# Kernel optimization log

Measured on AMD Instinct MI355X. Metric: run time of the kernel, lower is better.

Reference implementation:

```python
import jax, jax.numpy as jnp
import numpy as np

B, T, C = 2, 2048, 2048
H = 16
ROPE_DIM, NOPE_DIM, V_DIM = 64, 64, 128
HEAD_DIM = NOPE_DIM + ROPE_DIM  # 128
Q_RANK, KV_RANK = 1536, 512


def setup_inputs() -> dict:
    key = jax.random.key(0)
    ks = jax.random.split(key, 8)
    std = 0.02
    return {
        "x": jax.random.normal(ks[0], (B, T, C), jnp.float32),
        "cos": jax.random.normal(ks[1], (1, T, 1, ROPE_DIM // 2), jnp.float32),
        "sin": jax.random.normal(ks[2], (1, T, 1, ROPE_DIM // 2), jnp.float32),
        "wq_down": jax.random.normal(ks[3], (Q_RANK, C), jnp.float32) * std,
        "wq_up": jax.random.normal(ks[4], (H * HEAD_DIM, Q_RANK), jnp.float32) * std,
        "wkv_down": jax.random.normal(ks[5], (KV_RANK, C), jnp.float32) * std,
        "wkv_up": jax.random.normal(ks[6], (H * (HEAD_DIM + V_DIM), KV_RANK), jnp.float32) * std,
        "wo": jax.random.normal(ks[7], (C, H * V_DIM), jnp.float32) * std,
    }


def _rope(x, cos, sin):
    # x: [B, T, H, rope_dim]
    d = x.shape[-1] // 2
    x1, x2 = x[..., :d], x[..., d:]
    return jnp.concatenate([x1 * cos + x2 * sin, -x1 * sin + x2 * cos], axis=-1)


def _rms_norm(x):
    eps = jnp.finfo(x.dtype).eps
    return x * jax.lax.rsqrt(jnp.mean(jnp.square(x), axis=-1, keepdims=True) + eps)


def reference(x, cos, sin, wq_down, wq_up, wkv_down, wkv_up, wo):
    # Low-rank q projection
    q = jnp.einsum('btc,rc,dr->btd', x, wq_down, wq_up)
    q = q.reshape(B, T, H, HEAD_DIM)
    q_nope, q_rope = q[..., :NOPE_DIM], q[..., NOPE_DIM:]
    # Low-rank kv projection (naive decompression)
    kv = jnp.einsum('btc,rc,dr->btd', x, wkv_down, wkv_up)
    kv = kv.reshape(B, T, H, HEAD_DIM + V_DIM)
    k_nope = kv[..., :NOPE_DIM]
    k_rope = kv[..., NOPE_DIM:HEAD_DIM]
    v = kv[..., HEAD_DIM:]
    # Partial RoPE on the rope sub-dims only
    q_rope = _rope(q_rope, cos, sin)
    k_rope = _rope(k_rope, cos, sin)
    q = _rms_norm(jnp.concatenate([q_nope, q_rope], axis=-1))
    k = _rms_norm(jnp.concatenate([k_nope, k_rope], axis=-1))
    # Causal SDPA: [B, H, T, T]
    scale = 1.0 / jnp.sqrt(jnp.float32(HEAD_DIM))
    scores = jnp.einsum('bthd,bshd->bhts', q, k) * scale
    causal = jnp.tril(jnp.ones((T, T), dtype=bool))
    scores = jnp.where(causal, scores, jnp.finfo(scores.dtype).min)
    probs = jax.nn.softmax(scores, axis=-1)
    y = jnp.einsum('bhts,bshd->bthd', probs, v).reshape(B, T, H * V_DIM)
    return y @ wo.T
```

## Files before the change

kernel.cpp:

```cpp
#include <hip/hip_runtime.h>
#include <hip/hip_bf16.h>
#include <math.h>
#include <type_traits>

#define AS1 __attribute__((address_space(1)))
#define AS3 __attribute__((address_space(3)))

typedef __bf16  bf16x8 __attribute__((ext_vector_type(8)));
typedef float   f32x4  __attribute__((ext_vector_type(4)));
typedef __hip_bfloat16 bf16;

#define MFMA16x16x32 __builtin_amdgcn_mfma_f32_16x16x32_bf16

__device__ __forceinline__ void gload16(const void* g, void* l) {
  __builtin_amdgcn_global_load_lds((const AS1 void*)g, (AS3 void*)l, 16, 0, 0);
}

__device__ __forceinline__ unsigned short bfbits(float v) {
  return __builtin_bit_cast(unsigned short, __float2bfloat16(v));
}

struct CastArgs {
  const float4* src[6];
  ushort4* dst[6];
  unsigned bound[6];
};

__global__ __launch_bounds__(256) void f2bf_multi(CastArgs a) {
  unsigned i = blockIdx.x * 256 + threadIdx.x;
  if (i >= a.bound[5]) return;
  unsigned lo = 0;
  int s = 0;
#pragma unroll
  for (int k = 0; k < 5; k++) {
    if (i >= a.bound[k]) { s = k + 1; lo = a.bound[k]; }
  }
  unsigned idx = i - lo;
  float4 v = a.src[s][idx];
  ushort4 o;
  o.x = bfbits(v.x); o.y = bfbits(v.y); o.z = bfbits(v.z); o.w = bfbits(v.w);
  a.dst[s][idx] = o;
}

template <typename OutT>
__global__ __launch_bounds__(256, 3) void gemm_bt64(const bf16* __restrict__ A,
                                                    const bf16* __restrict__ W,
                                                    OutT* __restrict__ Cp,
                                                    int N, int K, int lda) {
  __shared__ __align__(16) bf16 As[128 * 64];
  __shared__ __align__(16) bf16 Ws[128 * 64];
  const int t = threadIdx.x;
  const int w = t >> 6, lane = t & 63;
  const int quad = lane >> 4, l16 = lane & 15;
  const int wr = (w >> 1) * 64, wc = (w & 1) * 64;
  const unsigned bid = blockIdx.x, nwg = gridDim.x;
  const unsigned swz = (bid & 7) * (nwg >> 3) + (bid >> 3);
  const size_t m0 = (size_t)(swz & 31) * 128;
  const size_t n0 = (size_t)(swz >> 5) * 128;

  const int r8 = lane >> 3;
  const int cg = (lane & 7) ^ r8;
  const bf16* aSrc = A + (m0 + w * 8 + r8) * (size_t)lda + cg * 8;
  const bf16* wSrc = W + (n0 + w * 8 + r8) * (size_t)K + cg * 8;
  const size_t sA = (size_t)32 * lda, sW = (size_t)32 * K;

  const int cx0 = ((quad) ^ (l16 & 7)) << 4;
  const int cx1 = ((4 + quad) ^ (l16 & 7)) << 4;
  const char* aRb = (const char*)As + (wr + l16) * 128;
  const char* bRb = (const char*)Ws + (wc + l16) * 128;

  f32x4 acc[4][4];
#pragma unroll
  for (int i = 0; i < 4; i++)
#pragma unroll
    for (int j = 0; j < 4; j++) acc[i][j] = f32x4{0.f, 0.f, 0.f, 0.f};

  for (int k0 = 0; k0 < K; k0 += 64) {
    __syncthreads();
#pragma unroll
    for (int is = 0; is < 4; ++is)
      gload16(aSrc + is * sA, (char*)As + is * 4096 + w * 1024);
#pragma unroll
    for (int is = 0; is < 4; ++is)
      gload16(wSrc + is * sW, (char*)Ws + is * 4096 + w * 1024);
    aSrc += 64; wSrc += 64;
    __syncthreads();

    bf16x8 af[4][2], bw[4][2];
#pragma unroll
    for (int i = 0; i < 4; i++) {
      af[i][0] = *(const bf16x8*)(aRb + i * 2048 + cx0);
      af[i][1] = *(const bf16x8*)(aRb + i * 2048 + cx1);
    }
#pragma unroll
    for (int j = 0; j < 4; j++) {
      bw[j][0] = *(const bf16x8*)(bRb + j * 2048 + cx0);
      bw[j][1] = *(const bf16x8*)(bRb + j * 2048 + cx1);
    }
    __builtin_amdgcn_s_setprio(1);
#pragma unroll
    for (int i = 0; i < 4; i++)
#pragma unroll
      for (int j = 0; j < 4; j++)
#pragma unroll
        for (int ks = 0; ks < 2; ks++)
          acc[i][j] = MFMA16x16x32(af[i][ks], bw[j][ks], acc[i][j], 0, 0, 0);
    __builtin_amdgcn_s_setprio(0);
  }

#pragma unroll
  for (int i = 0; i < 4; i++)
#pragma unroll
    for (int j = 0; j < 4; j++)
#pragma unroll
      for (int r = 0; r < 4; r++) {
        size_t row = m0 + wr + i * 16 + quad * 4 + r;
        size_t col = n0 + wc + j * 16 + l16;
        float v = acc[i][j][r];
        if constexpr (std::is_same<OutT, float>::value)
          Cp[row * N + col] = v;
        else
          Cp[row * N + col] = __float2bfloat16(v);
      }
}

__global__ __launch_bounds__(256, 3) void gemm_kvup64(const bf16* __restrict__ A,
                                                      const bf16* __restrict__ W,
                                                      bf16* __restrict__ kvraw,
                                                      bf16* __restrict__ vT) {
  __shared__ __align__(16) bf16 As[128 * 64];
  __shared__ __align__(16) bf16 Ws[128 * 64];
  const int t = threadIdx.x;
  const int w = t >> 6, lane = t & 63;
  const int quad = lane >> 4, l16 = lane & 15;
  const int wr = (w >> 1) * 64, wc = (w & 1) * 64;
  const int K = 512, lda = 2048;
  const unsigned bid = blockIdx.x, nwg = gridDim.x;
  const unsigned swz = (bid & 7) * (nwg >> 3) + (bid >> 3);
  const size_t m0 = (size_t)(swz & 31) * 128;
  const int n0 = (int)(swz >> 5) * 128;

  const int r8 = lane >> 3;
  const int cg = (lane & 7) ^ r8;
  const bf16* aSrc = A + (m0 + w * 8 + r8) * (size_t)lda + cg * 8;
  const bf16* wSrc = W + ((size_t)n0 + w * 8 + r8) * (size_t)K + cg * 8;
  const size_t sA = (size_t)32 * lda, sW = (size_t)32 * K;

  const int cx0 = ((quad) ^ (l16 & 7)) << 4;
  const int cx1 = ((4 + quad) ^ (l16 & 7)) << 4;
  const char* aRb = (const char*)As + (wr + l16) * 128;
  const char* bRb = (const char*)Ws + (wc + l16) * 128;

  f32x4 acc[4][4];
#pragma unroll
  for (int i = 0; i < 4; i++)
#pragma unroll
    for (int j = 0; j < 4; j++) acc[i][j] = f32x4{0.f, 0.f, 0.f, 0.f};

  for (int k0 = 0; k0 < K; k0 += 64) {
    __syncthreads();
#pragma unroll
    for (int is = 0; is < 4; ++is)
      gload16(aSrc + is * sA, (char*)As + is * 4096 + w * 1024);
#pragma unroll
    for (int is = 0; is < 4; ++is)
      gload16(wSrc + is * sW, (char*)Ws + is * 4096 + w * 1024);
    aSrc += 64; wSrc += 64;
    __syncthreads();

    bf16x8 af[4][2], bw[4][2];
#pragma unroll
    for (int i = 0; i < 4; i++) {
      af[i][0] = *(const bf16x8*)(aRb + i * 2048 + cx0);
      af[i][1] = *(const bf16x8*)(aRb + i * 2048 + cx1);
    }
#pragma unroll
    for (int j = 0; j < 4; j++) {
      bw[j][0] = *(const bf16x8*)(bRb + j * 2048 + cx0);
      bw[j][1] = *(const bf16x8*)(bRb + j * 2048 + cx1);
    }
    __builtin_amdgcn_s_setprio(1);
#pragma unroll
    for (int i = 0; i < 4; i++)
#pragma unroll
      for (int j = 0; j < 4; j++)
#pragma unroll
        for (int ks = 0; ks < 2; ks++)
          acc[i][j] = MFMA16x16x32(af[i][ks], bw[j][ks], acc[i][j], 0, 0, 0);
    __builtin_amdgcn_s_setprio(0);
  }

  if ((n0 & 128) == 0) {
#pragma unroll
    for (int i = 0; i < 4; i++)
#pragma unroll
      for (int j = 0; j < 4; j++)
#pragma unroll
        for (int r = 0; r < 4; r++) {
          size_t row = m0 + wr + i * 16 + quad * 4 + r;
          size_t col = (size_t)n0 + wc + j * 16 + l16;
          kvraw[row * 4096 + col] = __float2bfloat16(acc[i][j][r]);
        }
  } else {
    const int h = n0 >> 8;
#pragma unroll
    for (int i = 0; i < 4; i++) {
      size_t row = m0 + wr + i * 16 + quad * 4;
      int bb = (int)(row >> 11), tloc = (int)(row & 2047);
#pragma unroll
      for (int j = 0; j < 4; j++) {
        int d = wc + j * 16 + l16;
        ushort4 v4;
        v4.x = bfbits(acc[i][j][0]);
        v4.y = bfbits(acc[i][j][1]);
        v4.z = bfbits(acc[i][j][2]);
        v4.w = bfbits(acc[i][j][3]);
        *(ushort4*)(vT + ((size_t)(bb * 16 + h) * 128 + d) * 2048 + tloc) = v4;
      }
    }
  }
}

__global__ __launch_bounds__(256) void rope_rms(const bf16* __restrict__ qraw,
                                                const bf16* __restrict__ kvraw,
                                                const float* __restrict__ cosp,
                                                const float* __restrict__ sinp,
                                                bf16* __restrict__ qn,
                                                bf16* __restrict__ kn) {
  const int bt = blockIdx.x;
  const int w = threadIdx.x >> 6, lane = threadIdx.x & 63;
  const int h = blockIdx.y * 4 + w;
  const int tt = bt & 2047;
  const float c = cosp[tt * 32 + (lane & 31)];
  const float s = sinp[tt * 32 + (lane & 31)];
  const float inv128 = 1.0f / 128.0f;
  const float eps = 1.1920929e-7f;

  {
    const bf16* base = qraw + (size_t)bt * 2048 + h * 128;
    float a = (float)base[lane];
    float o = (float)base[64 + lane];
    float partner = __shfl_xor(o, 32);
    float orope = (lane < 32) ? (o * c + partner * s) : (o * c - partner * s);
    float ss = a * a + orope * orope;
#pragma unroll
    for (int off = 1; off < 64; off <<= 1) ss += __shfl_xor(ss, off);
    float rn = rsqrtf(ss * inv128 + eps);
    bf16* outp = qn + ((size_t)bt * 16 + h) * 128;
    outp[lane] = __float2bfloat16(a * rn);
    outp[64 + lane] = __float2bfloat16(orope * rn);
  }
  {
    const bf16* base = kvraw + (size_t)bt * 4096 + h * 256;
    float a = (float)base[lane];
    float o = (float)base[64 + lane];
    float partner = __shfl_xor(o, 32);
    float orope = (lane < 32) ? (o * c + partner * s) : (o * c - partner * s);
    float ss = a * a + orope * orope;
#pragma unroll
    for (int off = 1; off < 64; off <<= 1) ss += __shfl_xor(ss, off);
    float rn = rsqrtf(ss * inv128 + eps);
    bf16* outp = kn + ((size_t)bt * 16 + h) * 128;
    outp[lane] = __float2bfloat16(a * rn);
    outp[64 + lane] = __float2bfloat16(orope * rn);
  }
}

__global__ __launch_bounds__(256, 2) void attn_kernel(const bf16* __restrict__ qn,
                                                      const bf16* __restrict__ kn,
                                                      const bf16* __restrict__ vT,
                                                      bf16* __restrict__ y) {
  __shared__ __align__(16) bf16 Ks[2 * 64 * 128];
  __shared__ __align__(16) bf16 Vs[2 * 128 * 64];
  __shared__ __align__(16) bf16 Ps[4 * 16 * 64];
  const int t = threadIdx.x, w = t >> 6, lane = t & 63;
  const int quad = lane >> 4, l16 = lane & 15;
  const int b = blockIdx.x >> 4, h = blockIdx.x & 15;
  const int pr = (int)blockIdx.y;
  const int T_ = 2048, H_ = 16;
  const float K1 = 0.08838834764831845f * 1.4426950408889634f;
  const float K2 = -12.0f * 1.4426950408889634f;

  const int cgk = l16 ^ ((w * 4 + quad) & 7);
  const char* kg0 = (const char*)(kn + ((size_t)(b * T_) * H_ + h) * 128)
                    + (size_t)(w * 4 + quad) * 4096 + (size_t)cgk * 16;
  const int vrow = w * 8 + (lane >> 3);
  const int cgv = (lane & 7) ^ (vrow & 7);
  const char* vg0 = (const char*)(vT + ((size_t)(b * H_ + h) * 128 + vrow) * T_)
                    + (size_t)cgv * 16;

  auto stage = [&](auto bufc, int it2) {
    constexpr int BUF = decltype(bufc)::value;
    const size_t koff = (size_t)it2 * 262144;
    const size_t voff = (size_t)it2 * 128;
#pragma unroll
    for (int is = 0; is < 4; ++is)
      gload16(kg0 + koff + (size_t)is * 65536,
              (char*)Ks + BUF * 16384 + is * 4096 + w * 1024);
#pragma unroll
    for (int is = 0; is < 4; ++is)
      gload16(vg0 + voff + (size_t)is * 131072,
              (char*)Vs + BUF * 16384 + is * 4096 + w * 1024);
  };

  auto body = [&](auto bufc, int it, int nt, int xb,
                  bf16x8* qf, f32x4* yacc, float* lrow) {
    constexpr int BUF = decltype(bufc)::value;
    if (it + 1 < nt) {
      stage(std::integral_constant<int, 1 - BUF>{}, it + 1);
      __asm__ volatile("s_waitcnt vmcnt(8)" ::: "memory");
    } else {
      __asm__ volatile("s_waitcnt vmcnt(0)" ::: "memory");
    }
    __asm__ volatile("s_barrier" ::: "memory");

    f32x4 sacc[4];
#pragma unroll
    for (int cg = 0; cg < 4; cg++) sacc[cg] = f32x4{0.f, 0.f, 0.f, 0.f};
    __builtin_amdgcn_s_setprio(1);
#pragma unroll
    for (int cg = 0; cg < 4; ++cg) {
#pragma unroll
      for (int ks = 0; ks < 4; ++ks) {
        const int pos = (ks * 4 + quad) ^ (l16 & 7);
        const bf16x8 kf = *(const bf16x8*)((const char*)Ks + BUF * 16384 +
                                           (cg * 16 + l16) * 256 + pos * 16);
        sacc[cg] = MFMA16x16x32(qf[ks], kf, sacc[cg], 0, 0, 0);
      }
    }
    __builtin_amdgcn_s_setprio(0);

    const bool diag = (it == xb);
    float p[4][4];
#pragma unroll
    for (int cg = 0; cg < 4; ++cg)
#pragma unroll
      for (int r = 0; r < 4; ++r) {
        float e;
        if (diag && (cg * 16 + l16 > w * 16 + quad * 4 + r))
          e = 0.0f;
        else
          e = exp2f(fmaf(sacc[cg][r], K1, K2));
        p[cg][r] = e;
        lrow[r] += e;
      }

#pragma unroll
    for (int cg = 0; cg < 4; cg++)
#pragma unroll
      for (int r = 0; r < 4; r++) {
        const int row = quad * 4 + r;
        const int col = cg * 16 + l16;
        Ps[w * 1024 + row * 64 + (((col >> 3) ^ (row & 7)) << 3) + (col & 7)] =
            __float2bfloat16(p[cg][r]);
      }
    __asm__ volatile("s_waitcnt lgkmcnt(0)" ::: "memory");

    bf16x8 pf[2];
#pragma unroll
    for (int k2 = 0; k2 < 2; k2++)
      pf[k2] = *(const bf16x8*)(&Ps[w * 1024 + l16 * 64 +
                                    (((k2 * 4 + quad) ^ (l16 & 7)) << 3)]);
    __builtin_amdgcn_s_setprio(1);
#pragma unroll
    for (int dg = 0; dg < 8; dg++) {
#pragma unroll
      for (int k2 = 0; k2 < 2; k2++) {
        const int pos = (k2 * 4 + quad) ^ (l16 & 7);
        const bf16x8 vf = *(const bf16x8*)((const char*)Vs + BUF * 16384 +
                                           (dg * 16 + l16) * 128 + pos * 16);
        yacc[dg] = MFMA16x16x32(pf[k2], vf, yacc[dg], 0, 0, 0);
      }
    }
    __builtin_amdgcn_s_setprio(0);
    __asm__ volatile("s_barrier" ::: "memory");
  };

  const std::integral_constant<int, 0> c0{};
  const std::integral_constant<int, 1> c1{};

  for (int sidx = 0; sidx < 2; ++sidx) {
    const int xb = sidx ? pr : (31 - pr);
    const int q0 = xb * 64;
    const int nt = xb + 1;

    bf16x8 qf[4];
    {
      const bf16* qbase = qn + ((size_t)(b * T_ + q0 + w * 16 + l16) * H_ + h) * 128;
#pragma unroll
      for (int ks = 0; ks < 4; ks++) qf[ks] = *(const bf16x8*)(qbase + ks * 32 + quad * 8);
    }
    f32x4 yacc[8];
#pragma unroll
    for (int i = 0; i < 8; i++) yacc[i] = f32x4{0.f, 0.f, 0.f, 0.f};
    float lrow[4] = {0.f, 0.f, 0.f, 0.f};

    stage(c0, 0);
    int it = 0;
    for (; it + 2 <= nt; it += 2) {
      body(c0, it, nt, xb, qf, yacc, lrow);
      body(c1, it + 1, nt, xb, qf, yacc, lrow);
    }
    if (it < nt) body(c0, it, nt, xb, qf, yacc, lrow);

#pragma unroll
    for (int off = 1; off < 16; off <<= 1)
#pragma unroll
      for (int r = 0; r < 4; r++) lrow[r] += __shfl_xor(lrow[r], off);
#pragma unroll
    for (int r = 0; r < 4; r++) {
      float inv = 1.0f / lrow[r];
      size_t qrow = (size_t)(b * T_ + q0 + w * 16 + quad * 4 + r);
      bf16* outp = y + qrow * 2048 + h * 128;
#pragma unroll
      for (int dg = 0; dg < 8; dg++)
        outp[dg * 16 + l16] = __float2bfloat16(yacc[dg][r] * inv);
    }
  }
}

extern "C" void kernel_launch(void* const* d_in, const int* in_sizes, int n_in,
                              void* d_out, int out_size, void* d_ws, size_t ws_size,
                              hipStream_t stream) {
  (void)in_sizes; (void)n_in; (void)out_size; (void)ws_size;
  const float* x    = (const float*)d_in[0];
  const float* cosp = (const float*)d_in[1];
  const float* sinp = (const float*)d_in[2];
  const float* wqd  = (const float*)d_in[3];
  const float* wqu  = (const float*)d_in[4];
  const float* wkvd = (const float*)d_in[5];
  const float* wkvu = (const float*)d_in[6];
  const float* wo   = (const float*)d_in[7];
  float* out = (float*)d_out;

  char* ws = (char*)d_ws;
  size_t off = 0;
  auto alloc = [&](size_t elems) { bf16* p = (bf16*)(ws + off); off += elems * 2; return p; };
  bf16* xb      = alloc((size_t)4096 * 2048);
  bf16* wqdB    = alloc((size_t)1536 * 2048);
  bf16* wkvdB   = alloc((size_t)512 * 2048);
  bf16* wquB    = alloc((size_t)2048 * 1536);
  bf16* wkvuB   = alloc((size_t)4096 * 512);
  bf16* woB     = alloc((size_t)2048 * 2048);
  bf16* qkvdown = alloc((size_t)4096 * 2048);
  bf16* qraw    = alloc((size_t)4096 * 2048);
  bf16* kvraw   = alloc((size_t)4096 * 4096);
  bf16* qnb     = alloc((size_t)4096 * 16 * 128);
  bf16* knb     = alloc((size_t)4096 * 16 * 128);
  bf16* vTb     = alloc((size_t)2 * 16 * 128 * 2048);
  bf16* yb      = alloc((size_t)4096 * 2048);

  CastArgs ca;
  const float* srcs[6] = {x, wqd, wkvd, wqu, wkvu, wo};
  bf16* dsts[6]        = {xb, wqdB, wkvdB, wquB, wkvuB, woB};
  size_t cnts[6] = {(size_t)4096 * 2048, (size_t)1536 * 2048, (size_t)512 * 2048,
                    (size_t)2048 * 1536, (size_t)4096 * 512,  (size_t)2048 * 2048};
  unsigned cum = 0;
  for (int i = 0; i < 6; i++) {
    ca.src[i] = (const float4*)srcs[i];
    ca.dst[i] = (ushort4*)dsts[i];
    cum += (unsigned)(cnts[i] / 4);
    ca.bound[i] = cum;
  }
  f2bf_multi<<<dim3((cum + 255) / 256), 256, 0, stream>>>(ca);

  gemm_bt64<bf16><<<dim3(512), 256, 0, stream>>>(xb, wqdB, qkvdown, 2048, 2048, 2048);
  gemm_bt64<bf16><<<dim3(512), 256, 0, stream>>>(qkvdown, wquB, qraw, 2048, 1536, 2048);
  gemm_kvup64<<<dim3(1024), 256, 0, stream>>>(qkvdown + 1536, wkvuB, kvraw, vTb);
  rope_rms<<<dim3(4096, 4), 256, 0, stream>>>(qraw, kvraw, cosp, sinp, qnb, knb);
  attn_kernel<<<dim3(32, 16), 256, 0, stream>>>(qnb, knb, vTb, yb);
  gemm_bt64<float><<<dim3(512), 256, 0, stream>>>(yb, woB, out, 2048, 2048, 2048);
}
```

Measured before the change: 369.3 us.

## Shrink attention KV tile to 32 and give each block one query tile

The attention kernel now streams K/V in 32-key tiles instead of 64, which halves shared memory per block, and raises launch bounds to 4 blocks per CU. The grid is doubled so each block handles a single 64-row query tile instead of a pair. The block-to-tile mapping is arranged in four groups so that long and short causal rows are interleaved for load balance. The goal is higher occupancy and better latency hiding, at the cost of twice as many iterations, more barriers, smaller MFMA batches per tile, and reloading Q per block.

```diff
diff --git a/kernel.cpp b/kernel.cpp
--- a/kernel.cpp
+++ b/kernel.cpp
@@ -266,17 +266,26 @@
   }
 }
 
-__global__ __launch_bounds__(256, 2) void attn_kernel(const bf16* __restrict__ qn,
+__global__ __launch_bounds__(256, 4) void attn_kernel(const bf16* __restrict__ qn,
                                                       const bf16* __restrict__ kn,
                                                       const bf16* __restrict__ vT,
                                                       bf16* __restrict__ y) {
-  __shared__ __align__(16) bf16 Ks[2 * 64 * 128];
-  __shared__ __align__(16) bf16 Vs[2 * 128 * 64];
-  __shared__ __align__(16) bf16 Ps[4 * 16 * 64];
+  __shared__ __align__(16) bf16 Ks[2 * 32 * 128];
+  __shared__ __align__(16) bf16 Vs[2 * 128 * 32];
+  __shared__ __align__(16) bf16 Ps[4 * 16 * 32];
   const int t = threadIdx.x, w = t >> 6, lane = t & 63;
   const int quad = lane >> 4, l16 = lane & 15;
   const int b = blockIdx.x >> 4, h = blockIdx.x & 15;
-  const int pr = (int)blockIdx.y;
+  const int yy = (int)blockIdx.y;
+  const int y0 = yy & 7, k4 = yy >> 3;
+  int xb;
+  if (k4 == 0) xb = 31 - y0;
+  else if (k4 == 1) xb = y0;
+  else if (k4 == 2) xb = 23 - y0;
+  else xb = 8 + y0;
+  const int q0 = xb * 64;
+  const int nt = 2 * xb + 2;
+  const int it2x = 2 * xb;
   const int T_ = 2048, H_ = 16;
   const float K1 = 0.08838834764831845f * 1.4426950408889634f;
   const float K2 = -12.0f * 1.4426950408889634f;
@@ -284,60 +293,60 @@
   const int cgk = l16 ^ ((w * 4 + quad) & 7);
   const char* kg0 = (const char*)(kn + ((size_t)(b * T_) * H_ + h) * 128)
                     + (size_t)(w * 4 + quad) * 4096 + (size_t)cgk * 16;
-  const int vrow = w * 8 + (lane >> 3);
-  const int cgv = (lane & 7) ^ (vrow & 7);
+  const int vrow = w * 16 + (lane >> 2);
+  const int cgv = (lane & 3) ^ ((lane >> 2) & 3);
   const char* vg0 = (const char*)(vT + ((size_t)(b * H_ + h) * 128 + vrow) * T_)
                     + (size_t)cgv * 16;
 
   auto stage = [&](auto bufc, int it2) {
     constexpr int BUF = decltype(bufc)::value;
-    const size_t koff = (size_t)it2 * 262144;
-    const size_t voff = (size_t)it2 * 128;
-#pragma unroll
-    for (int is = 0; is < 4; ++is)
+    const size_t koff = (size_t)it2 * 131072;
+    const size_t voff = (size_t)it2 * 64;
+#pragma unroll
+    for (int is = 0; is < 2; ++is)
       gload16(kg0 + koff + (size_t)is * 65536,
-              (char*)Ks + BUF * 16384 + is * 4096 + w * 1024);
-#pragma unroll
-    for (int is = 0; is < 4; ++is)
-      gload16(vg0 + voff + (size_t)is * 131072,
-              (char*)Vs + BUF * 16384 + is * 4096 + w * 1024);
+              (char*)Ks + BUF * 8192 + is * 4096 + w * 1024);
+#pragma unroll
+    for (int is = 0; is < 2; ++is)
+      gload16(vg0 + voff + (size_t)is * 262144,
+              (char*)Vs + BUF * 8192 + is * 4096 + w * 1024);
   };
 
-  auto body = [&](auto bufc, int it, int nt, int xb,
-                  bf16x8* qf, f32x4* yacc, float* lrow) {
+  auto body = [&](auto bufc, int it, bf16x8* qf, f32x4* yacc, float* lrow) {
     constexpr int BUF = decltype(bufc)::value;
     if (it + 1 < nt) {
       stage(std::integral_constant<int, 1 - BUF>{}, it + 1);
-      __asm__ volatile("s_waitcnt vmcnt(8)" ::: "memory");
+      __asm__ volatile("s_waitcnt vmcnt(4)" ::: "memory");
     } else {
       __asm__ volatile("s_waitcnt vmcnt(0)" ::: "memory");
     }
     __asm__ volatile("s_barrier" ::: "memory");
 
-    f32x4 sacc[4];
-#pragma unroll
-    for (int cg = 0; cg < 4; cg++) sacc[cg] = f32x4{0.f, 0.f, 0.f, 0.f};
+    f32x4 sacc[2];
+#pragma unroll
+    for (int cg = 0; cg < 2; cg++) sacc[cg] = f32x4{0.f, 0.f, 0.f, 0.f};
     __builtin_amdgcn_s_setprio(1);
 #pragma unroll
-    for (int cg = 0; cg < 4; ++cg) {
+    for (int cg = 0; cg < 2; ++cg) {
 #pragma unroll
       for (int ks = 0; ks < 4; ++ks) {
         const int pos = (ks * 4 + quad) ^ (l16 & 7);
-        const bf16x8 kf = *(const bf16x8*)((const char*)Ks + BUF * 16384 +
+        const bf16x8 kf = *(const bf16x8*)((const char*)Ks + BUF * 8192 +
                                            (cg * 16 + l16) * 256 + pos * 16);
         sacc[cg] = MFMA16x16x32(qf[ks], kf, sacc[cg], 0, 0, 0);
       }
     }
     __builtin_amdgcn_s_setprio(0);
 
-    const bool diag = (it == xb);
-    float p[4][4];
-#pragma unroll
-    for (int cg = 0; cg < 4; ++cg)
+    const bool diag = (it >= it2x);
+    const int soff = (it - it2x) * 32;
+    float p[2][4];
+#pragma unroll
+    for (int cg = 0; cg < 2; ++cg)
 #pragma unroll
       for (int r = 0; r < 4; ++r) {
         float e;
-        if (diag && (cg * 16 + l16 > w * 16 + quad * 4 + r))
+        if (diag && (soff + cg * 16 + l16 > w * 16 + quad * 4 + r))
           e = 0.0f;
         else
           e = exp2f(fmaf(sacc[cg][r], K1, K2));
@@ -346,31 +355,25 @@
       }
 
 #pragma unroll
-    for (int cg = 0; cg < 4; cg++)
+    for (int cg = 0; cg < 2; cg++)
 #pragma unroll
       for (int r = 0; r < 4; r++) {
         const int row = quad * 4 + r;
         const int col = cg * 16 + l16;
-        Ps[w * 1024 + row * 64 + (((col >> 3) ^ (row & 7)) << 3) + (col & 7)] =
+        Ps[w * 512 + row * 32 + (((col >> 3) ^ (row & 3)) << 3) + (col & 7)] =
             __float2bfloat16(p[cg][r]);
       }
     __asm__ volatile("s_waitcnt lgkmcnt(0)" ::: "memory");
 
-    bf16x8 pf[2];
-#pragma unroll
-    for (int k2 = 0; k2 < 2; k2++)
-      pf[k2] = *(const bf16x8*)(&Ps[w * 1024 + l16 * 64 +
-                                    (((k2 * 4 + quad) ^ (l16 & 7)) << 3)]);
+    const bf16x8 pf = *(const bf16x8*)(&Ps[w * 512 + l16 * 32 +
+                                           ((quad ^ (l16 & 3)) << 3)]);
     __builtin_amdgcn_s_setprio(1);
 #pragma unroll
     for (int dg = 0; dg < 8; dg++) {
-#pragma unroll
-      for (int k2 = 0; k2 < 2; k2++) {
-        const int pos = (k2 * 4 + quad) ^ (l16 & 7);
-        const bf16x8 vf = *(const bf16x8*)((const char*)Vs + BUF * 16384 +
-                                           (dg * 16 + l16) * 128 + pos * 16);
-        yacc[dg] = MFMA16x16x32(pf[k2], vf, yacc[dg], 0, 0, 0);
-      }
+      const int pos = quad ^ (l16 & 3);
+      const bf16x8 vf = *(const bf16x8*)((const char*)Vs + BUF * 8192 +
+                                         (dg * 16 + l16) * 64 + pos * 16);
+      yacc[dg] = MFMA16x16x32(pf, vf, yacc[dg], 0, 0, 0);
     }
     __builtin_amdgcn_s_setprio(0);
     __asm__ volatile("s_barrier" ::: "memory");
@@ -379,43 +382,35 @@
   const std::integral_constant<int, 0> c0{};
   const std::integral_constant<int, 1> c1{};
 
-  for (int sidx = 0; sidx < 2; ++sidx) {
-    const int xb = sidx ? pr : (31 - pr);
-    const int q0 = xb * 64;
-    const int nt = xb + 1;
-
-    bf16x8 qf[4];
-    {
-      const bf16* qbase = qn + ((size_t)(b * T_ + q0 + w * 16 + l16) * H_ + h) * 128;
-#pragma unroll
-      for (int ks = 0; ks < 4; ks++) qf[ks] = *(const bf16x8*)(qbase + ks * 32 + quad * 8);
-    }
-    f32x4 yacc[8];
-#pragma unroll
-    for (int i = 0; i < 8; i++) yacc[i] = f32x4{0.f, 0.f, 0.f, 0.f};
-    float lrow[4] = {0.f, 0.f, 0.f, 0.f};
-
-    stage(c0, 0);
-    int it = 0;
-    for (; it + 2 <= nt; it += 2) {
-      body(c0, it, nt, xb, qf, yacc, lrow);
-      body(c1, it + 1, nt, xb, qf, yacc, lrow);
-    }
-    if (it < nt) body(c0, it, nt, xb, qf, yacc, lrow);
-
-#pragma unroll
-    for (int off = 1; off < 16; off <<= 1)
-#pragma unroll
-      for (int r = 0; r < 4; r++) lrow[r] += __shfl_xor(lrow[r], off);
-#pragma unroll
-    for (int r = 0; r < 4; r++) {
-      float inv = 1.0f / lrow[r];
-      size_t qrow = (size_t)(b * T_ + q0 + w * 16 + quad * 4 + r);
-      bf16* outp = y + qrow * 2048 + h * 128;
-#pragma unroll
-      for (int dg = 0; dg < 8; dg++)
-        outp[dg * 16 + l16] = __float2bfloat16(yacc[dg][r] * inv);
-    }
+  bf16x8 qf[4];
+  {
+    const bf16* qbase = qn + ((size_t)(b * T_ + q0 + w * 16 + l16) * H_ + h) * 128;
+#pragma unroll
+    for (int ks = 0; ks < 4; ks++) qf[ks] = *(const bf16x8*)(qbase + ks * 32 + quad * 8);
+  }
+  f32x4 yacc[8];
+#pragma unroll
+  for (int i = 0; i < 8; i++) yacc[i] = f32x4{0.f, 0.f, 0.f, 0.f};
+  float lrow[4] = {0.f, 0.f, 0.f, 0.f};
+
+  stage(c0, 0);
+  for (int it = 0; it < nt; it += 2) {
+    body(c0, it, qf, yacc, lrow);
+    body(c1, it + 1, qf, yacc, lrow);
+  }
+
+#pragma unroll
+  for (int off = 1; off < 16; off <<= 1)
+#pragma unroll
+    for (int r = 0; r < 4; r++) lrow[r] += __shfl_xor(lrow[r], off);
+#pragma unroll
+  for (int r = 0; r < 4; r++) {
+    float inv = 1.0f / lrow[r];
+    size_t qrow = (size_t)(b * T_ + q0 + w * 16 + quad * 4 + r);
+    bf16* outp = y + qrow * 2048 + h * 128;
+#pragma unroll
+    for (int dg = 0; dg < 8; dg++)
+      outp[dg * 16 + l16] = __float2bfloat16(yacc[dg][r] * inv);
   }
 }
 
@@ -468,6 +463,6 @@
   gemm_bt64<bf16><<<dim3(512), 256, 0, stream>>>(qkvdown, wquB, qraw, 2048, 1536, 2048);
   gemm_kvup64<<<dim3(1024), 256, 0, stream>>>(qkvdown + 1536, wkvuB, kvraw, vTb);
   rope_rms<<<dim3(4096, 4), 256, 0, stream>>>(qraw, kvraw, cosp, sinp, qnb, knb);
-  attn_kernel<<<dim3(32, 16), 256, 0, stream>>>(qnb, knb, vTb, yb);
+  attn_kernel<<<dim3(32, 32), 256, 0, stream>>>(qnb, knb, vTb, yb);
   gemm_bt64<float><<<dim3(512), 256, 0, stream>>>(yb, woB, out, 2048, 2048, 2048);
 }
```

New measurement: 381.3 us. 3.2% more time.
